# Kernel tuning notes

Measured on AMD Instinct MI355X. Metric: run time of the kernel, lower is better.

The kernel has to match this reference:

```python
import jax, jax.numpy as jnp
import numpy as np

D_MODEL = 1024
N_HEAD = 16
D_HEAD = D_MODEL // N_HEAD
EXP = 4
B, T = 2, 2048
EPS = 1e-5

def setup_inputs() -> dict:
    key = jax.random.key(0)
    ks = jax.random.split(key, 16)
    s = 0.02
    return {
        "x": jax.random.normal(ks[0], (B, T, D_MODEL), jnp.float32),
        "ln1_w": jnp.ones((D_MODEL,), jnp.float32),
        "ln1_b": jnp.zeros((D_MODEL,), jnp.float32),
        "attn_w": jax.random.normal(ks[1], (D_MODEL, 3 * D_MODEL), jnp.float32) * s,
        "attn_b": jnp.zeros((3 * D_MODEL,), jnp.float32),
        "proj_w": jax.random.normal(ks[2], (D_MODEL, D_MODEL), jnp.float32) * s,
        "proj_b": jnp.zeros((D_MODEL,), jnp.float32),
        "ln2_w": jnp.ones((D_MODEL,), jnp.float32),
        "ln2_b": jnp.zeros((D_MODEL,), jnp.float32),
        "fc_w": jax.random.normal(ks[3], (D_MODEL, EXP * D_MODEL), jnp.float32) * s,
        "fc_b": jnp.zeros((EXP * D_MODEL,), jnp.float32),
        "fc2_w": jax.random.normal(ks[4], (EXP * D_MODEL, D_MODEL), jnp.float32) * s,
        "fc2_b": jnp.zeros((D_MODEL,), jnp.float32),
    }

def _layernorm(x, w, b):
    mu = jnp.mean(x, axis=-1, keepdims=True)
    var = jnp.mean(jnp.square(x - mu), axis=-1, keepdims=True)
    return (x - mu) * jax.lax.rsqrt(var + EPS) * w + b

def _attn(x, attn_w, attn_b, proj_w, proj_b):
    Bx, Tx, C = x.shape
    qkv = x @ attn_w + attn_b  # [B,T,3C]
    q, k, v = jnp.split(qkv, 3, axis=-1)
    # [B, H, T, Dh]
    q = q.reshape(Bx, Tx, N_HEAD, D_HEAD).transpose(0, 2, 1, 3)
    k = k.reshape(Bx, Tx, N_HEAD, D_HEAD).transpose(0, 2, 1, 3)
    v = v.reshape(Bx, Tx, N_HEAD, D_HEAD).transpose(0, 2, 1, 3)
    att = jnp.einsum('bhqd,bhkd->bhqk', q, k) * (1.0 / np.sqrt(D_HEAD))
    causal = jnp.tril(jnp.ones((Tx, Tx), bool))
    att = jnp.where(causal, att, -jnp.inf)
    att = jax.nn.softmax(att, axis=-1)
    y = jnp.einsum('bhqk,bhkd->bhqd', att, v)
    y = y.transpose(0, 2, 1, 3).reshape(Bx, Tx, C)
    return y @ proj_w + proj_b

def reference(x, ln1_w, ln1_b, attn_w, attn_b, proj_w, proj_b,
              ln2_w, ln2_b, fc_w, fc_b, fc2_w, fc2_b):
    x = x + _attn(_layernorm(x, ln1_w, ln1_b), attn_w, attn_b, proj_w, proj_b)
    h = _layernorm(x, ln2_w, ln2_b)
    h = jax.nn.gelu(h @ fc_w + fc_b, approximate=False)  # exact GELU (torch nn.GELU default)
    x = x + (h @ fc2_w + fc2_b)
    return x
```

## Files before the change

### kernel.cpp

```cpp
#include <hip/hip_runtime.h>
#include <hip/hip_bf16.h>
#include <math.h>


#define D_MODEL 1024
#define N_HEAD  16
#define D_HEAD  64
#define SEQ_T   2048
#define BATCH   2
#define NROWS   (BATCH * SEQ_T)
#define C3      (3 * D_MODEL)
#define D_FF    (4 * D_MODEL)

typedef __bf16 bf16x8 __attribute__((ext_vector_type(8)));
typedef __bf16 bf16x4t __attribute__((ext_vector_type(4)));
typedef short  s16x4  __attribute__((ext_vector_type(4)));
typedef float  f32x4  __attribute__((ext_vector_type(4)));

#define WAIT_VM0() asm volatile("s_waitcnt vmcnt(0)" ::: "memory")
#define WAIT_VM2() asm volatile("s_waitcnt vmcnt(2)" ::: "memory")
#define WAIT_VM4() asm volatile("s_waitcnt vmcnt(4)" ::: "memory")

__device__ __forceinline__ f32x4 mfma16_bf16(s16x4 a, s16x4 b, f32x4 c)
{
#if __has_builtin(__builtin_amdgcn_mfma_f32_16x16x16_bf16)
    return __builtin_amdgcn_mfma_f32_16x16x16_bf16(
        __builtin_bit_cast(bf16x4t, a), __builtin_bit_cast(bf16x4t, b), c, 0, 0, 0);
#else
    return __builtin_amdgcn_mfma_f32_16x16x16bf16_1k(a, b, c, 0, 0, 0);
#endif
}

__global__ __launch_bounds__(256) void ln_kernel(
    const float* __restrict__ in, const float* __restrict__ w,
    const float* __restrict__ b, __hip_bfloat16* __restrict__ out, int D)
{
    const int row = blockIdx.x;
    const int tid = threadIdx.x;
    const float* x = in + (size_t)row * 1024;

    const float4 v = *(const float4*)(x + tid * 4);
    float s  = v.x + v.y + v.z + v.w;
    float s2 = v.x * v.x + v.y * v.y + v.z * v.z + v.w * v.w;

    __shared__ float rs[256], rs2[256];
    rs[tid] = s; rs2[tid] = s2;
    __syncthreads();
    for (int off = 128; off > 0; off >>= 1) {
        if (tid < off) { rs[tid] += rs[tid + off]; rs2[tid] += rs2[tid + off]; }
        __syncthreads();
    }
    const float mu   = rs[0] * (1.0f / 1024.0f);
    const float var  = rs2[0] * (1.0f / 1024.0f) - mu * mu;
    const float rstd = rsqrtf(var + 1e-5f);

    const float4 w4 = *(const float4*)(w + tid * 4);
    const float4 b4 = *(const float4*)(b + tid * 4);
    float o[4] = {(v.x - mu) * rstd * w4.x + b4.x,
                  (v.y - mu) * rstd * w4.y + b4.y,
                  (v.z - mu) * rstd * w4.z + b4.z,
                  (v.w - mu) * rstd * w4.w + b4.w};
    ushort4 pk;
    { __hip_bfloat16 e0 = __float2bfloat16(o[0]); pk.x = *(unsigned short*)&e0;
      __hip_bfloat16 e1 = __float2bfloat16(o[1]); pk.y = *(unsigned short*)&e1;
      __hip_bfloat16 e2 = __float2bfloat16(o[2]); pk.z = *(unsigned short*)&e2;
      __hip_bfloat16 e3 = __float2bfloat16(o[3]); pk.w = *(unsigned short*)&e3; }
    *(ushort4*)(out + (size_t)row * 1024 + tid * 4) = pk;
}

__global__ __launch_bounds__(256) void transpose_all_kernel(
    const float* __restrict__ attn_w, const float* __restrict__ proj_w,
    const float* __restrict__ fc_w,   const float* __restrict__ fc2_w,
    __hip_bfloat16* __restrict__ attn_wt, __hip_bfloat16* __restrict__ proj_wt,
    __hip_bfloat16* __restrict__ fc_wt,   __hip_bfloat16* __restrict__ fc2_wt)
{
    __shared__ float t[32][33];
    int tb = blockIdx.x;
    const float* W; __hip_bfloat16* Wt; int K, N;
    if (tb < 3072)      { W = attn_w; Wt = attn_wt; K = D_MODEL; N = C3; }
    else if (tb < 4096) { tb -= 3072; W = proj_w; Wt = proj_wt; K = D_MODEL; N = D_MODEL; }
    else if (tb < 8192) { tb -= 4096; W = fc_w;   Wt = fc_wt;   K = D_MODEL; N = D_FF; }
    else                { tb -= 8192; W = fc2_w;  Wt = fc2_wt;  K = D_FF;    N = D_MODEL; }
    const int ntx = N >> 5;
    const int k0 = (tb / ntx) * 32;
    const int n0 = (tb % ntx) * 32;

    const int row = threadIdx.x >> 3;
    const int c4  = (threadIdx.x & 7) * 4;

    const float4 v = *(const float4*)&W[(size_t)(k0 + row) * N + n0 + c4];
    t[row][c4 + 0] = v.x; t[row][c4 + 1] = v.y;
    t[row][c4 + 2] = v.z; t[row][c4 + 3] = v.w;
    __syncthreads();

    ushort4 pk;
    { __hip_bfloat16 e0 = __float2bfloat16(t[c4 + 0][row]); pk.x = *(unsigned short*)&e0;
      __hip_bfloat16 e1 = __float2bfloat16(t[c4 + 1][row]); pk.y = *(unsigned short*)&e1;
      __hip_bfloat16 e2 = __float2bfloat16(t[c4 + 2][row]); pk.z = *(unsigned short*)&e2;
      __hip_bfloat16 e3 = __float2bfloat16(t[c4 + 3][row]); pk.w = *(unsigned short*)&e3; }
    *(ushort4*)&Wt[(size_t)(n0 + row) * K + k0 + c4] = pk;
}

__device__ __forceinline__ void async16(const __hip_bfloat16* g, __hip_bfloat16* l)
{
    __builtin_amdgcn_global_load_lds(
        (const __attribute__((address_space(1))) void*)g,
        (__attribute__((address_space(3))) void*)l, 16, 0, 0);
}

__device__ __forceinline__ float gelu_fast(float v)
{
    const float t = v * (0.7978845608f + 0.0356774081f * v * v);
    return v / (1.0f + exp2f(-2.885390082f * t));
}

__device__ __forceinline__ void swz_xcd(int& bx, int& by)
{
    const int nbx = gridDim.x;
    const int nwg = nbx * gridDim.y;
    int lin = blockIdx.y * nbx + blockIdx.x;
    const int per = nwg >> 3;
    lin = (lin & 7) * per + (lin >> 3);
    bx = lin % nbx;
    by = lin / nbx;
}


__device__ __forceinline__ void gemm8p_core(
    const __hip_bfloat16* __restrict__ A,
    const __hip_bfloat16* __restrict__ Bt,
    int K, int row0, int col0, f32x4 (&acc)[8][4],
    __hip_bfloat16 (*Asl)[4][64 * 64], __hip_bfloat16 (*Bsl)[2][128 * 64])
{
    const int tid  = threadIdx.x;
    const int wv   = tid >> 6;
    const int lane = tid & 63;
    const int ln15 = lane & 15;
    const int lq   = lane >> 4;
    const int wr   = wv >> 2;
    const int wc   = wv & 3;

    const int srow = tid >> 3;
    const int sg   = ((tid & 7) ^ ((tid >> 3) & 7)) * 8;
    const __hip_bfloat16* Ab = A  + (size_t)(row0 + srow) * K + sg;
    const __hip_bfloat16* Bb = Bt + (size_t)(col0 + srow) * K + sg;
    const int nt = K >> 6;

#pragma unroll
    for (int mi = 0; mi < 8; ++mi)
#pragma unroll
        for (int ni = 0; ni < 4; ++ni) acc[mi][ni] = (f32x4){0.f, 0.f, 0.f, 0.f};

    auto stA = [&](int t, int buf, int b) {
        async16(Ab + (size_t)(b * 64) * K + t * 64, &Asl[buf][b][0] + tid * 8);
    };
    auto stB = [&](int t, int buf, int h) {
        async16(Bb + (size_t)(h * 128) * K + t * 64, &Bsl[buf][h][0] + tid * 8);
        async16(Bb + (size_t)(h * 128 + 64) * K + t * 64,
                &Bsl[buf][h][0] + 4096 + tid * 8);
    };

    const int rg0 = (lq ^ (ln15 & 7)) * 8;
    const int rg1 = ((4 | lq) ^ (ln15 & 7)) * 8;
    auto ldA = [&](int buf, int mi, int kk) -> bf16x8 {
        return *(const bf16x8*)&Asl[buf][wr * 2 + (mi >> 2)]
            [((mi & 3) * 16 + ln15) * 64 + (kk ? rg1 : rg0)];
    };
    auto ldB = [&](int buf, int ni, int kk) -> bf16x8 {
        return *(const bf16x8*)&Bsl[buf][wc >> 1]
            [((wc & 1) * 64 + ni * 16 + ln15) * 64 + (kk ? rg1 : rg0)];
    };

    stB(0, 0, 0); stB(0, 0, 1);
    stA(0, 0, 0); stA(0, 0, 2); stA(0, 0, 1); stA(0, 0, 3);
    WAIT_VM0();
    __builtin_amdgcn_s_barrier();

    for (int t = 0; t < nt; ++t) {
        const int pp = t & 1, op = pp ^ 1;
        const int tc = (t + 1 < nt) ? t + 1 : nt - 1;
        bf16x8 af[2][2], bfr[4][2];

#pragma unroll
        for (int m = 0; m < 2; ++m) { af[m][0] = ldA(pp, m, 0); af[m][1] = ldA(pp, m, 1); }
#pragma unroll
        for (int ni = 0; ni < 4; ++ni) { bfr[ni][0] = ldB(pp, ni, 0); bfr[ni][1] = ldB(pp, ni, 1); }
        stB(tc, op, 0);
        __builtin_amdgcn_s_barrier();
        __builtin_amdgcn_s_setprio(1);
#pragma unroll
        for (int kk = 0; kk < 2; ++kk)
#pragma unroll
            for (int m = 0; m < 2; ++m)
#pragma unroll
                for (int ni = 0; ni < 4; ++ni)
                    acc[m][ni] = __builtin_amdgcn_mfma_f32_16x16x32_bf16(
                        af[m][kk], bfr[ni][kk], acc[m][ni], 0, 0, 0);
        __builtin_amdgcn_s_setprio(0);
        __builtin_amdgcn_s_barrier();

#pragma unroll
        for (int m = 0; m < 2; ++m) { af[m][0] = ldA(pp, 2 + m, 0); af[m][1] = ldA(pp, 2 + m, 1); }
        stB(tc, op, 1);
        WAIT_VM4();
        __builtin_amdgcn_s_barrier();
        __builtin_amdgcn_s_setprio(1);
#pragma unroll
        for (int kk = 0; kk < 2; ++kk)
#pragma unroll
            for (int m = 0; m < 2; ++m)
#pragma unroll
                for (int ni = 0; ni < 4; ++ni)
                    acc[2 + m][ni] = __builtin_amdgcn_mfma_f32_16x16x32_bf16(
                        af[m][kk], bfr[ni][kk], acc[2 + m][ni], 0, 0, 0);
        __builtin_amdgcn_s_setprio(0);
        __builtin_amdgcn_s_barrier();

#pragma unroll
        for (int m = 0; m < 2; ++m) { af[m][0] = ldA(pp, 4 + m, 0); af[m][1] = ldA(pp, 4 + m, 1); }
        stA(tc, op, 0); stA(tc, op, 2);
        __builtin_amdgcn_s_barrier();
        __builtin_amdgcn_s_setprio(1);
#pragma unroll
        for (int kk = 0; kk < 2; ++kk)
#pragma unroll
            for (int m = 0; m < 2; ++m)
#pragma unroll
                for (int ni = 0; ni < 4; ++ni)
                    acc[4 + m][ni] = __builtin_amdgcn_mfma_f32_16x16x32_bf16(
                        af[m][kk], bfr[ni][kk], acc[4 + m][ni], 0, 0, 0);
        __builtin_amdgcn_s_setprio(0);
        __builtin_amdgcn_s_barrier();

#pragma unroll
        for (int m = 0; m < 2; ++m) { af[m][0] = ldA(pp, 6 + m, 0); af[m][1] = ldA(pp, 6 + m, 1); }
        stA(tc, op, 1); stA(tc, op, 3);
        WAIT_VM2();
        __builtin_amdgcn_s_barrier();
        __builtin_amdgcn_s_setprio(1);
#pragma unroll
        for (int kk = 0; kk < 2; ++kk)
#pragma unroll
            for (int m = 0; m < 2; ++m)
#pragma unroll
                for (int ni = 0; ni < 4; ++ni)
                    acc[6 + m][ni] = __builtin_amdgcn_mfma_f32_16x16x32_bf16(
                        af[m][kk], bfr[ni][kk], acc[6 + m][ni], 0, 0, 0);
        __builtin_amdgcn_s_setprio(0);
        __builtin_amdgcn_s_barrier();
    }
}

__global__ __launch_bounds__(512, 1) void gemm8p_kernel(
    const __hip_bfloat16* __restrict__ A,
    const __hip_bfloat16* __restrict__ Bt,
    const float* __restrict__ bias,
    __hip_bfloat16* __restrict__ Cout,
    int M, int N, int K, int act)
{
    __shared__ __align__(16) __hip_bfloat16 Asl[2][4][64 * 64];
    __shared__ __align__(16) __hip_bfloat16 Bsl[2][2][128 * 64];

    int bx, by;
    swz_xcd(bx, by);
    const int row0 = by * 256;
    const int col0 = bx * 256;

    f32x4 acc[8][4];
    gemm8p_core(A, Bt, K, row0, col0, acc, Asl, Bsl);

    const int tid  = threadIdx.x;
    const int wv   = tid >> 6;
    const int lane = tid & 63;
    const int ln15 = lane & 15;
    const int lq   = lane >> 4;
    const int mbase = (wv >> 2) * 128;
    const int nbase = (wv & 3) * 64;

#pragma unroll
    for (int mi = 0; mi < 8; ++mi) {
#pragma unroll
        for (int ni = 0; ni < 4; ++ni) {
            const int gc = col0 + nbase + ni * 16 + ln15;
            const float bv = bias[gc];
#pragma unroll
            for (int r = 0; r < 4; ++r) {
                const int gr = row0 + mbase + mi * 16 + lq * 4 + r;
                float v = acc[mi][ni][r] + bv;
                if (act == 1) v = gelu_fast(v);
                Cout[(size_t)gr * N + gc] = __float2bfloat16(v);
            }
        }
    }
}

__global__ __launch_bounds__(512, 1) void qkv8p_kernel(
    const __hip_bfloat16* __restrict__ A,
    const __hip_bfloat16* __restrict__ Bt,
    const float* __restrict__ bias,
    __hip_bfloat16* __restrict__ Qb,
    __hip_bfloat16* __restrict__ Kb,
    __hip_bfloat16* __restrict__ Vtb)
{
    __shared__ __align__(16) __hip_bfloat16 Asl[2][4][64 * 64];
    __shared__ __align__(16) __hip_bfloat16 Bsl[2][2][128 * 64];

    int bx, by;
    swz_xcd(bx, by);
    const int row0 = by * 256;
    const int col0 = bx * 256;

    f32x4 acc[8][4];
    gemm8p_core(A, Bt, D_MODEL, row0, col0, acc, Asl, Bsl);

    const int tid  = threadIdx.x;
    const int wv   = tid >> 6;
    const int lane = tid & 63;
    const int ln15 = lane & 15;
    const int lq   = lane >> 4;
    const int mbase = (wv >> 2) * 128;
    const int nbase = (wv & 3) * 64;

#pragma unroll
    for (int mi = 0; mi < 8; ++mi) {
        const int gr0 = row0 + mbase + mi * 16 + lq * 4;
        const int bb  = gr0 >> 11;
        const int q0  = gr0 & 2047;
#pragma unroll
        for (int ni = 0; ni < 4; ++ni) {
            const int gc  = col0 + nbase + ni * 16 + ln15;
            const float bv = bias[gc];
            const int sec = gc >> 10;
            const int hd  = (gc & 1023) >> 6;
            const int d   = gc & 63;
            if (sec == 2) {
                unsigned short u[4];
#pragma unroll
                for (int r = 0; r < 4; ++r) {
                    __hip_bfloat16 e = __float2bfloat16(acc[mi][ni][r] + bv);
                    u[r] = *(unsigned short*)&e;
                }
                uint2 pk;
                pk.x = (unsigned int)u[0] | ((unsigned int)u[1] << 16);
                pk.y = (unsigned int)u[2] | ((unsigned int)u[3] << 16);
                *(uint2*)(Vtb + ((size_t)((bb * N_HEAD + hd) * D_HEAD + d)) * SEQ_T + q0) = pk;
            } else {
                __hip_bfloat16* dst = (sec == 0 ? Qb : Kb)
                    + ((size_t)((bb * N_HEAD + hd) * SEQ_T + q0)) * D_HEAD + d;
#pragma unroll
                for (int r = 0; r < 4; ++r)
                    dst[(size_t)r * D_HEAD] = __float2bfloat16(acc[mi][ni][r] + bv);
            }
        }
    }
}

__device__ __forceinline__ void stage_db2w(
    const __hip_bfloat16* __restrict__ Ab, const __hip_bfloat16* __restrict__ Bb,
    int K, int kt, __hip_bfloat16* __restrict__ as,
    __hip_bfloat16* __restrict__ bs, int tid)
{
    const int k0 = kt * 64;
#pragma unroll
    for (int s = 0; s < 2; ++s) {
        async16(Ab + k0 + s * 32, as + s * 64 * 32 + tid * 8);
#pragma unroll
        for (int i = 0; i < 2; ++i)
            async16(Bb + (size_t)(i * 64) * K + k0 + s * 32,
                    bs + s * 128 * 32 + i * 64 * 32 + tid * 8);
    }
}

__device__ __forceinline__ void gemm_db2w(
    const __hip_bfloat16* __restrict__ A,
    const __hip_bfloat16* __restrict__ Bt,
    int K, int row0, int col0, f32x4 (&acc)[2][4])
{
    __shared__ __align__(16) __hip_bfloat16 Asl[2][2 * 64 * 32];
    __shared__ __align__(16) __hip_bfloat16 Bsl[2][2 * 128 * 32];

    const int tid  = threadIdx.x;
    const int wv   = tid >> 6;
    const int lane = tid & 63;
    const int ln15 = lane & 15;
    const int lq   = lane >> 4;
    const int mbase = (wv >> 1) * 32;
    const int nbase = (wv & 1) * 64;
    const int rcol = (lq ^ ((ln15 >> 1) & 3)) * 8;
    const int ssw  = ((tid & 3) ^ ((tid >> 3) & 3)) * 8;
    const __hip_bfloat16* Ab = A  + (size_t)(row0 + (tid >> 2)) * K + ssw;
    const __hip_bfloat16* Bb = Bt + (size_t)(col0 + (tid >> 2)) * K + ssw;
    const int nt = K >> 6;

#pragma unroll
    for (int mi = 0; mi < 2; ++mi)
#pragma unroll
        for (int ni = 0; ni < 4; ++ni) acc[mi][ni] = (f32x4){0.f, 0.f, 0.f, 0.f};

    stage_db2w(Ab, Bb, K, 0, &Asl[0][0], &Bsl[0][0], tid);
    WAIT_VM0();
    __builtin_amdgcn_s_barrier();

    for (int t = 0; t < nt; ++t) {
        const int p   = t & 1;
        const int tcl = (t + 1 < nt) ? t + 1 : nt - 1;
        bf16x8 af[2][2], bfr[2][4];

#pragma unroll
        for (int s = 0; s < 2; ++s) {
#pragma unroll
            for (int mi = 0; mi < 2; ++mi)
                af[s][mi] = *(const bf16x8*)
                    &Asl[p][s * 64 * 32 + (mbase + mi * 16 + ln15) * 32 + rcol];
#pragma unroll
            for (int ni = 0; ni < 4; ++ni)
                bfr[s][ni] = *(const bf16x8*)
                    &Bsl[p][s * 128 * 32 + (nbase + ni * 16 + ln15) * 32 + rcol];
        }

        stage_db2w(Ab, Bb, K, tcl, &Asl[p ^ 1][0], &Bsl[p ^ 1][0], tid);

        __builtin_amdgcn_s_setprio(1);
#pragma unroll
        for (int s = 0; s < 2; ++s)
#pragma unroll
            for (int mi = 0; mi < 2; ++mi)
#pragma unroll
                for (int ni = 0; ni < 4; ++ni)
                    acc[mi][ni] = __builtin_amdgcn_mfma_f32_16x16x32_bf16(
                        af[s][mi], bfr[s][ni], acc[mi][ni], 0, 0, 0);
        __builtin_amdgcn_s_setprio(0);

        WAIT_VM0();
        __builtin_amdgcn_s_barrier();
    }
}

__global__ __launch_bounds__(256, 3) void gemm64_kernel(
    const __hip_bfloat16* __restrict__ A,
    const __hip_bfloat16* __restrict__ Bt,
    const float* __restrict__ bias,
    const float* __restrict__ residual,
    void* __restrict__ Cout,
    int M, int N, int K, int act, int outBf16)
{
    int bx, by;
    swz_xcd(bx, by);
    const int row0 = by * 64;
    const int col0 = bx * 128;

    f32x4 acc[2][4];
    gemm_db2w(A, Bt, K, row0, col0, acc);

    const int tid  = threadIdx.x;
    const int wv   = tid >> 6;
    const int lane = tid & 63;
    const int ln15 = lane & 15;
    const int lq   = lane >> 4;
    const int mbase = (wv >> 1) * 32;
    const int nbase = (wv & 1) * 64;

#pragma unroll
    for (int mi = 0; mi < 2; ++mi) {
#pragma unroll
        for (int ni = 0; ni < 4; ++ni) {
            const int gc = col0 + nbase + ni * 16 + ln15;
            const float bv = bias[gc];
#pragma unroll
            for (int r = 0; r < 4; ++r) {
                const int gr = row0 + mbase + mi * 16 + lq * 4 + r;
                float v = acc[mi][ni][r] + bv;
                if (act == 1) v = gelu_fast(v);
                if (residual) v += residual[(size_t)gr * N + gc];
                if (outBf16)
                    ((__hip_bfloat16*)Cout)[(size_t)gr * N + gc] = __float2bfloat16(v);
                else
                    ((float*)Cout)[(size_t)gr * N + gc] = v;
            }
        }
    }
}

#define ATQ 64
#define ATK 128
#define NQT (SEQ_T / ATQ)
#define VP2 136

__global__ __launch_bounds__(256) void mfma_attn_kernel(
    const __hip_bfloat16* __restrict__ Qb,
    const __hip_bfloat16* __restrict__ Kb,
    const __hip_bfloat16* __restrict__ Vtb,
    __hip_bfloat16* __restrict__ y)
{
    __shared__ __align__(16) __hip_bfloat16 Ks[2 * ATK * 32];
    __shared__ __align__(16) __hip_bfloat16 Vts[D_HEAD * VP2];

    const int flat = (blockIdx.z * gridDim.y + blockIdx.y) * gridDim.x + blockIdx.x;
    const int xcd  = flat & 7;
    const int slot = flat >> 3;
    const int pair = slot & 15;
    const int hb   = slot >> 4;
    const int h    = xcd + 8 * (hb & 1);
    const int b    = hb >> 1;

    const int tid  = threadIdx.x;
    const int wv   = tid >> 6;
    const int lane = tid & 63;
    const int ln15 = lane & 15;
    const int lq   = lane >> 4;

    const __hip_bfloat16* Qh = Qb  + (size_t)(b * N_HEAD + h) * SEQ_T * D_HEAD;
    const __hip_bfloat16* Kh = Kb  + (size_t)(b * N_HEAD + h) * SEQ_T * D_HEAD;
    const __hip_bfloat16* Vh = Vtb + (size_t)(b * N_HEAD + h) * D_HEAD * SEQ_T;
    const size_t bT = (size_t)b * SEQ_T;

    const float CEXP = 0.18033688011f;
    const float DTHR = 8.0f / CEXP;

    bf16x8 kreg[4], vreg[4];
    const int kr = tid >> 3, kg = tid & 7;
    const int vr = tid >> 4, vc = tid & 15;
    const int khalf = kg >> 2;
    const int kpos  = (kg & 3) ^ ((kr >> 1) & 3);

    auto issue = [&](int kb) {
#pragma unroll
        for (int i = 0; i < 4; ++i)
            kreg[i] = *(const bf16x8*)(Kh + (size_t)(kb + kr + i * 32) * D_HEAD + kg * 8);
#pragma unroll
        for (int i = 0; i < 4; ++i)
            vreg[i] = *(const bf16x8*)(Vh + (size_t)(vr + i * 16) * SEQ_T + kb + vc * 8);
    };
    auto commit = [&]() {
#pragma unroll
        for (int i = 0; i < 4; ++i) {
            const int r = kr + i * 32;
            *(bf16x8*)&Ks[khalf * (ATK * 32) + r * 32 + kpos * 8] = kreg[i];
        }
#pragma unroll
        for (int i = 0; i < 4; ++i) {
            const int r = vr + i * 16;
            *(bf16x8*)&Vts[r * VP2 + vc * 8] = vreg[i];
        }
    };

    const int rcol = (lq ^ ((ln15 >> 1) & 3)) * 8;

#pragma unroll 1
    for (int half = 0; half < 2; ++half) {
        const int qt    = half == 0 ? pair : (NQT - 1 - pair);
        const int qbase = qt * ATQ;
        const int ntk   = (qt >> 1) + 1;
        const int qg    = qbase + wv * 16 + ln15;

        bf16x8 qf[2];
#pragma unroll
        for (int kc = 0; kc < 2; ++kc)
            qf[kc] = *(const bf16x8*)(Qh + (size_t)(qbase + wv * 16 + ln15) * D_HEAD
                                      + kc * 32 + lq * 8);

        f32x4 Oacc[4];
#pragma unroll
        for (int dn = 0; dn < 4; ++dn) Oacc[dn] = (f32x4){0.f, 0.f, 0.f, 0.f};
        float m_run = -INFINITY, l_run = 0.f;

        issue(0);

        for (int t = 0; t < ntk; ++t) {
            const int kb = t * ATK;
            commit();
            __syncthreads();
            if (t + 1 < ntk) issue((t + 1) * ATK);

            f32x4 st[8];
#pragma unroll
            for (int jf = 0; jf < 8; ++jf) st[jf] = (f32x4){0.f, 0.f, 0.f, 0.f};
            __builtin_amdgcn_s_setprio(1);
#pragma unroll
            for (int jf = 0; jf < 8; ++jf) {
                const int rw = jf * 16 + ln15;
                const bf16x8 kf0 = *(const bf16x8*)&Ks[rw * 32 + rcol];
                const bf16x8 kf1 = *(const bf16x8*)&Ks[ATK * 32 + rw * 32 + rcol];
                st[jf] = __builtin_amdgcn_mfma_f32_16x16x32_bf16(kf0, qf[0], st[jf], 0, 0, 0);
                st[jf] = __builtin_amdgcn_mfma_f32_16x16x32_bf16(kf1, qf[1], st[jf], 0, 0, 0);
            }
            __builtin_amdgcn_s_setprio(0);

            if (t == ntk - 1) {
#pragma unroll
                for (int jf = 0; jf < 8; ++jf)
#pragma unroll
                    for (int r = 0; r < 4; ++r)
                        if ((kb + jf * 16 + lq * 4 + r) > qg) st[jf][r] = -INFINITY;
            }

            float tmax = st[0][0];
#pragma unroll
            for (int jf = 0; jf < 8; ++jf)
#pragma unroll
                for (int r = 0; r < 4; ++r) tmax = fmaxf(tmax, st[jf][r]);
            tmax = fmaxf(tmax, __shfl_xor(tmax, 16));
            tmax = fmaxf(tmax, __shfl_xor(tmax, 32));

            if (!__all(tmax <= m_run + DTHR)) {
                const float mnew  = fmaxf(m_run, tmax);
                const float alpha = exp2f((m_run - mnew) * CEXP);
                l_run *= alpha;
                m_run = mnew;
                float a4[4];
#pragma unroll
                for (int r = 0; r < 4; ++r) a4[r] = __shfl(alpha, lq * 4 + r);
#pragma unroll
                for (int dn = 0; dn < 4; ++dn)
#pragma unroll
                    for (int r = 0; r < 4; ++r) Oacc[dn][r] *= a4[r];
            }
            const float mc = m_run * CEXP;
            float psum = 0.f;
#pragma unroll
            for (int jf = 0; jf < 8; ++jf)
#pragma unroll
                for (int r = 0; r < 4; ++r) {
                    const float p = exp2f(fmaf(st[jf][r], CEXP, -mc));
                    st[jf][r] = p;
                    psum += p;
                }
            psum += __shfl_xor(psum, 16);
            psum += __shfl_xor(psum, 32);
            l_run += psum;

            __builtin_amdgcn_s_setprio(1);
#pragma unroll
            for (int jf = 0; jf < 8; ++jf) {
                s16x4 pfr;
#pragma unroll
                for (int s = 0; s < 4; ++s) {
                    __hip_bfloat16 e = __float2bfloat16(st[jf][s]);
                    pfr[s] = __builtin_bit_cast(short, e);
                }
#pragma unroll
                for (int dn = 0; dn < 4; ++dn) {
                    const s16x4 vfr = *(const s16x4*)&Vts[(dn * 16 + ln15) * VP2
                                                          + jf * 16 + lq * 4];
                    Oacc[dn] = mfma16_bf16(pfr, vfr, Oacc[dn]);
                }
            }
            __builtin_amdgcn_s_setprio(0);
            __syncthreads();
        }

        float il[4];
#pragma unroll
        for (int r = 0; r < 4; ++r) il[r] = 1.0f / __shfl(l_run, lq * 4 + r);
#pragma unroll
        for (int dn = 0; dn < 4; ++dn)
#pragma unroll
            for (int r = 0; r < 4; ++r)
                Ks[(wv * 16 + lq * 4 + r) * 72 + dn * 16 + ln15] =
                    __float2bfloat16(Oacc[dn][r] * il[r]);
        const int r2 = lane >> 3, c8 = (lane & 7) * 8;
#pragma unroll
        for (int i = 0; i < 2; ++i) {
            const int row = wv * 16 + r2 + 8 * i;
            const bf16x8 val = *(const bf16x8*)&Ks[row * 72 + c8];
            *(bf16x8*)(y + (bT + qbase + row) * D_MODEL + h * D_HEAD + c8) = val;
        }
        __syncthreads();
    }
}

extern "C" void kernel_launch(void* const* d_in, const int* in_sizes, int n_in,
                              void* d_out, int out_size, void* d_ws, size_t ws_size,
                              hipStream_t stream)
{
    const float* x      = (const float*)d_in[0];
    const float* ln1_w  = (const float*)d_in[1];
    const float* ln1_b  = (const float*)d_in[2];
    const float* attn_w = (const float*)d_in[3];
    const float* attn_b = (const float*)d_in[4];
    const float* proj_w = (const float*)d_in[5];
    const float* proj_b = (const float*)d_in[6];
    const float* ln2_w  = (const float*)d_in[7];
    const float* ln2_b  = (const float*)d_in[8];
    const float* fc_w   = (const float*)d_in[9];
    const float* fc_b   = (const float*)d_in[10];
    const float* fc2_w  = (const float*)d_in[11];
    const float* fc2_b  = (const float*)d_in[12];
    float* out = (float*)d_out;

    char* ws = (char*)d_ws;
    __hip_bfloat16* Qb      = (__hip_bfloat16*)(ws);
    __hip_bfloat16* Kb      = (__hip_bfloat16*)(ws + (size_t)8  * 1024 * 1024);
    __hip_bfloat16* Vtb     = (__hip_bfloat16*)(ws + (size_t)16 * 1024 * 1024);
    __hip_bfloat16* h_bf    = (__hip_bfloat16*)(ws);
    __hip_bfloat16* ln_buf  = (__hip_bfloat16*)(ws + (size_t)32 * 1024 * 1024);
    __hip_bfloat16* y_buf   = (__hip_bfloat16*)(ws + (size_t)40 * 1024 * 1024);
    float*          xmid    = (float*)(ws + (size_t)48 * 1024 * 1024);
    __hip_bfloat16* attn_wt = (__hip_bfloat16*)(ws + (size_t)64 * 1024 * 1024);
    __hip_bfloat16* proj_wt = (__hip_bfloat16*)(ws + (size_t)70 * 1024 * 1024);
    __hip_bfloat16* fc_wt   = (__hip_bfloat16*)(ws + (size_t)72 * 1024 * 1024);
    __hip_bfloat16* fc2_wt  = (__hip_bfloat16*)(ws + (size_t)80 * 1024 * 1024);

    dim3 blk256(256);
    dim3 blk512(512);

    transpose_all_kernel<<<dim3(12288), blk256, 0, stream>>>(
        attn_w, proj_w, fc_w, fc2_w, attn_wt, proj_wt, fc_wt, fc2_wt);

    ln_kernel<<<dim3(NROWS), blk256, 0, stream>>>(x, ln1_w, ln1_b, ln_buf, D_MODEL);

    qkv8p_kernel<<<dim3(C3 / 256, NROWS / 256), blk512, 0, stream>>>(
        ln_buf, attn_wt, attn_b, Qb, Kb, Vtb);

    mfma_attn_kernel<<<dim3(NQT / 2, N_HEAD, BATCH), blk256, 0, stream>>>(
        Qb, Kb, Vtb, y_buf);

    gemm64_kernel<<<dim3(D_MODEL / 128, NROWS / 64), blk256, 0, stream>>>(
        y_buf, proj_wt, proj_b, x, xmid, NROWS, D_MODEL, D_MODEL, 0, 0);

    ln_kernel<<<dim3(NROWS), blk256, 0, stream>>>(xmid, ln2_w, ln2_b, ln_buf, D_MODEL);

    gemm8p_kernel<<<dim3(D_FF / 256, NROWS / 256), blk512, 0, stream>>>(
        ln_buf, fc_wt, fc_b, h_bf, NROWS, D_FF, D_MODEL, 1);

    gemm64_kernel<<<dim3(D_MODEL / 128, NROWS / 64), blk256, 0, stream>>>(
        h_bf, fc2_wt, fc2_b, xmid, out, NROWS, D_MODEL, D_FF, 0, 0);
}
```

Measured before the change: 339.7 us.

## Split-K the fc2 GEMM with atomics and fuse LN1 into weight prep

The fc2 GEMM (K=4096) now runs as a two-way split-K grid. Each half atomically adds its partial sum into the output. That output is pre-initialized by the proj epilogue to xmid + fc2_b, which moves the fc2 bias and residual out of the fc2 kernel. The split is meant to fill more of the GPU, since 512 blocks underfill the CUs, at the cost of float atomics and an extra 16MB output write in proj. Separately, the LN1 pass is folded into the weight transpose kernel as extra blocks, removing one launch.

```diff
diff --git a/kernel.cpp b/kernel.cpp
--- a/kernel.cpp
+++ b/kernel.cpp
@@ -68,14 +68,51 @@
     *(ushort4*)(out + (size_t)row * 1024 + tid * 4) = pk;
 }
 
-__global__ __launch_bounds__(256) void transpose_all_kernel(
+__global__ __launch_bounds__(256) void prep_kernel(
     const float* __restrict__ attn_w, const float* __restrict__ proj_w,
     const float* __restrict__ fc_w,   const float* __restrict__ fc2_w,
     __hip_bfloat16* __restrict__ attn_wt, __hip_bfloat16* __restrict__ proj_wt,
-    __hip_bfloat16* __restrict__ fc_wt,   __hip_bfloat16* __restrict__ fc2_wt)
-{
-    __shared__ float t[32][33];
+    __hip_bfloat16* __restrict__ fc_wt,   __hip_bfloat16* __restrict__ fc2_wt,
+    const float* __restrict__ x, const float* __restrict__ ln1_w,
+    const float* __restrict__ ln1_b, __hip_bfloat16* __restrict__ ln_out)
+{
+    __shared__ float smem[32 * 33];
     int tb = blockIdx.x;
+    const int tid = threadIdx.x;
+
+    if (tb >= 12288) {
+        const int row = tb - 12288;
+        const float* xr = x + (size_t)row * 1024;
+        const float4 v = *(const float4*)(xr + tid * 4);
+        float s  = v.x + v.y + v.z + v.w;
+        float s2 = v.x * v.x + v.y * v.y + v.z * v.z + v.w * v.w;
+        float* rs  = smem;
+        float* rs2 = smem + 256;
+        rs[tid] = s; rs2[tid] = s2;
+        __syncthreads();
+        for (int off = 128; off > 0; off >>= 1) {
+            if (tid < off) { rs[tid] += rs[tid + off]; rs2[tid] += rs2[tid + off]; }
+            __syncthreads();
+        }
+        const float mu   = rs[0] * (1.0f / 1024.0f);
+        const float var  = rs2[0] * (1.0f / 1024.0f) - mu * mu;
+        const float rstd = rsqrtf(var + 1e-5f);
+        const float4 w4 = *(const float4*)(ln1_w + tid * 4);
+        const float4 b4 = *(const float4*)(ln1_b + tid * 4);
+        float o[4] = {(v.x - mu) * rstd * w4.x + b4.x,
+                      (v.y - mu) * rstd * w4.y + b4.y,
+                      (v.z - mu) * rstd * w4.z + b4.z,
+                      (v.w - mu) * rstd * w4.w + b4.w};
+        ushort4 pk;
+        { __hip_bfloat16 e0 = __float2bfloat16(o[0]); pk.x = *(unsigned short*)&e0;
+          __hip_bfloat16 e1 = __float2bfloat16(o[1]); pk.y = *(unsigned short*)&e1;
+          __hip_bfloat16 e2 = __float2bfloat16(o[2]); pk.z = *(unsigned short*)&e2;
+          __hip_bfloat16 e3 = __float2bfloat16(o[3]); pk.w = *(unsigned short*)&e3; }
+        *(ushort4*)(ln_out + (size_t)row * 1024 + tid * 4) = pk;
+        return;
+    }
+
+    float (*t)[33] = (float(*)[33])smem;
     const float* W; __hip_bfloat16* Wt; int K, N;
     if (tb < 3072)      { W = attn_w; Wt = attn_wt; K = D_MODEL; N = C3; }
     else if (tb < 4096) { tb -= 3072; W = proj_w; Wt = proj_wt; K = D_MODEL; N = D_MODEL; }
@@ -85,8 +122,8 @@
     const int k0 = (tb / ntx) * 32;
     const int n0 = (tb % ntx) * 32;
 
-    const int row = threadIdx.x >> 3;
-    const int c4  = (threadIdx.x & 7) * 4;
+    const int row = tid >> 3;
+    const int c4  = (tid & 7) * 4;
 
     const float4 v = *(const float4*)&W[(size_t)(k0 + row) * N + n0 + c4];
     t[row][c4 + 0] = v.x; t[row][c4 + 1] = v.y;
@@ -357,7 +394,7 @@
 
 __device__ __forceinline__ void stage_db2w(
     const __hip_bfloat16* __restrict__ Ab, const __hip_bfloat16* __restrict__ Bb,
-    int K, int kt, __hip_bfloat16* __restrict__ as,
+    int Kst, int kt, __hip_bfloat16* __restrict__ as,
     __hip_bfloat16* __restrict__ bs, int tid)
 {
     const int k0 = kt * 64;
@@ -366,7 +403,7 @@
         async16(Ab + k0 + s * 32, as + s * 64 * 32 + tid * 8);
 #pragma unroll
         for (int i = 0; i < 2; ++i)
-            async16(Bb + (size_t)(i * 64) * K + k0 + s * 32,
+            async16(Bb + (size_t)(i * 64) * Kst + k0 + s * 32,
                     bs + s * 128 * 32 + i * 64 * 32 + tid * 8);
     }
 }
@@ -374,7 +411,7 @@
 __device__ __forceinline__ void gemm_db2w(
     const __hip_bfloat16* __restrict__ A,
     const __hip_bfloat16* __restrict__ Bt,
-    int K, int row0, int col0, f32x4 (&acc)[2][4])
+    int Kst, int Kext, int row0, int col0, f32x4 (&acc)[2][4])
 {
     __shared__ __align__(16) __hip_bfloat16 Asl[2][2 * 64 * 32];
     __shared__ __align__(16) __hip_bfloat16 Bsl[2][2 * 128 * 32];
@@ -388,16 +425,16 @@
     const int nbase = (wv & 1) * 64;
     const int rcol = (lq ^ ((ln15 >> 1) & 3)) * 8;
     const int ssw  = ((tid & 3) ^ ((tid >> 3) & 3)) * 8;
-    const __hip_bfloat16* Ab = A  + (size_t)(row0 + (tid >> 2)) * K + ssw;
-    const __hip_bfloat16* Bb = Bt + (size_t)(col0 + (tid >> 2)) * K + ssw;
-    const int nt = K >> 6;
+    const __hip_bfloat16* Ab = A  + (size_t)(row0 + (tid >> 2)) * Kst + ssw;
+    const __hip_bfloat16* Bb = Bt + (size_t)(col0 + (tid >> 2)) * Kst + ssw;
+    const int nt = Kext >> 6;
 
 #pragma unroll
     for (int mi = 0; mi < 2; ++mi)
 #pragma unroll
         for (int ni = 0; ni < 4; ++ni) acc[mi][ni] = (f32x4){0.f, 0.f, 0.f, 0.f};
 
-    stage_db2w(Ab, Bb, K, 0, &Asl[0][0], &Bsl[0][0], tid);
+    stage_db2w(Ab, Bb, Kst, 0, &Asl[0][0], &Bsl[0][0], tid);
     WAIT_VM0();
     __builtin_amdgcn_s_barrier();
 
@@ -418,7 +455,7 @@
                     &Bsl[p][s * 128 * 32 + (nbase + ni * 16 + ln15) * 32 + rcol];
         }
 
-        stage_db2w(Ab, Bb, K, tcl, &Asl[p ^ 1][0], &Bsl[p ^ 1][0], tid);
+        stage_db2w(Ab, Bb, Kst, tcl, &Asl[p ^ 1][0], &Bsl[p ^ 1][0], tid);
 
         __builtin_amdgcn_s_setprio(1);
 #pragma unroll
@@ -436,13 +473,15 @@
     }
 }
 
-__global__ __launch_bounds__(256, 3) void gemm64_kernel(
+__global__ __launch_bounds__(256, 3) void proj_kernel(
     const __hip_bfloat16* __restrict__ A,
     const __hip_bfloat16* __restrict__ Bt,
     const float* __restrict__ bias,
     const float* __restrict__ residual,
-    void* __restrict__ Cout,
-    int M, int N, int K, int act, int outBf16)
+    float* __restrict__ Xmid,
+    float* __restrict__ OutInit,
+    const float* __restrict__ bias2,
+    int M, int N, int K)
 {
     int bx, by;
     swz_xcd(bx, by);
@@ -450,7 +489,7 @@
     const int col0 = bx * 128;
 
     f32x4 acc[2][4];
-    gemm_db2w(A, Bt, K, row0, col0, acc);
+    gemm_db2w(A, Bt, K, K, row0, col0, acc);
 
     const int tid  = threadIdx.x;
     const int wv   = tid >> 6;
@@ -465,17 +504,51 @@
 #pragma unroll
         for (int ni = 0; ni < 4; ++ni) {
             const int gc = col0 + nbase + ni * 16 + ln15;
-            const float bv = bias[gc];
+            const float bv  = bias[gc];
+            const float bv2 = bias2[gc];
 #pragma unroll
             for (int r = 0; r < 4; ++r) {
                 const int gr = row0 + mbase + mi * 16 + lq * 4 + r;
-                float v = acc[mi][ni][r] + bv;
-                if (act == 1) v = gelu_fast(v);
-                if (residual) v += residual[(size_t)gr * N + gc];
-                if (outBf16)
-                    ((__hip_bfloat16*)Cout)[(size_t)gr * N + gc] = __float2bfloat16(v);
-                else
-                    ((float*)Cout)[(size_t)gr * N + gc] = v;
+                const float v = acc[mi][ni][r] + bv + residual[(size_t)gr * N + gc];
+                Xmid[(size_t)gr * N + gc]    = v;
+                OutInit[(size_t)gr * N + gc] = v + bv2;
+            }
+        }
+    }
+}
+
+__global__ __launch_bounds__(256, 3) void fc2s_kernel(
+    const __hip_bfloat16* __restrict__ A,
+    const __hip_bfloat16* __restrict__ Bt,
+    float* __restrict__ Out,
+    int M, int N, int K)
+{
+    const int split = blockIdx.z;
+    int bx, by;
+    swz_xcd(bx, by);
+    const int row0 = by * 64;
+    const int col0 = bx * 128;
+
+    f32x4 acc[2][4];
+    gemm_db2w(A + split * (K / 2), Bt + split * (K / 2), K, K / 2, row0, col0, acc);
+
+    const int tid  = threadIdx.x;
+    const int wv   = tid >> 6;
+    const int lane = tid & 63;
+    const int ln15 = lane & 15;
+    const int lq   = lane >> 4;
+    const int mbase = (wv >> 1) * 32;
+    const int nbase = (wv & 1) * 64;
+
+#pragma unroll
+    for (int mi = 0; mi < 2; ++mi) {
+#pragma unroll
+        for (int ni = 0; ni < 4; ++ni) {
+            const int gc = col0 + nbase + ni * 16 + ln15;
+#pragma unroll
+            for (int r = 0; r < 4; ++r) {
+                const int gr = row0 + mbase + mi * 16 + lq * 4 + r;
+                atomicAdd(&Out[(size_t)gr * N + gc], acc[mi][ni][r]);
             }
         }
     }
@@ -704,10 +777,9 @@
     dim3 blk256(256);
     dim3 blk512(512);
 
-    transpose_all_kernel<<<dim3(12288), blk256, 0, stream>>>(
-        attn_w, proj_w, fc_w, fc2_w, attn_wt, proj_wt, fc_wt, fc2_wt);
-
-    ln_kernel<<<dim3(NROWS), blk256, 0, stream>>>(x, ln1_w, ln1_b, ln_buf, D_MODEL);
+    prep_kernel<<<dim3(12288 + NROWS), blk256, 0, stream>>>(
+        attn_w, proj_w, fc_w, fc2_w, attn_wt, proj_wt, fc_wt, fc2_wt,
+        x, ln1_w, ln1_b, ln_buf);
 
     qkv8p_kernel<<<dim3(C3 / 256, NROWS / 256), blk512, 0, stream>>>(
         ln_buf, attn_wt, attn_b, Qb, Kb, Vtb);
@@ -715,14 +787,15 @@
     mfma_attn_kernel<<<dim3(NQT / 2, N_HEAD, BATCH), blk256, 0, stream>>>(
         Qb, Kb, Vtb, y_buf);
 
-    gemm64_kernel<<<dim3(D_MODEL / 128, NROWS / 64), blk256, 0, stream>>>(
-        y_buf, proj_wt, proj_b, x, xmid, NROWS, D_MODEL, D_MODEL, 0, 0);
+    proj_kernel<<<dim3(D_MODEL / 128, NROWS / 64), blk256, 0, stream>>>(
+        y_buf, proj_wt, proj_b, x, xmid, out, fc2_b,
+        NROWS, D_MODEL, D_MODEL);
 
     ln_kernel<<<dim3(NROWS), blk256, 0, stream>>>(xmid, ln2_w, ln2_b, ln_buf, D_MODEL);
 
     gemm8p_kernel<<<dim3(D_FF / 256, NROWS / 256), blk512, 0, stream>>>(
         ln_buf, fc_wt, fc_b, h_bf, NROWS, D_FF, D_MODEL, 1);
 
-    gemm64_kernel<<<dim3(D_MODEL / 128, NROWS / 64), blk256, 0, stream>>>(
-        h_bf, fc2_wt, fc2_b, xmid, out, NROWS, D_MODEL, D_FF, 0, 0);
-}
+    fc2s_kernel<<<dim3(D_MODEL / 128, NROWS / 64, 2), blk256, 0, stream>>>(
+        h_bf, fc2_wt, out, NROWS, D_MODEL, D_FF);
+}
```

New measurement: 345.3 us. Within noise of the previous version (+1.7%).
